# Kernel optimization log

Measured on AMD Instinct MI355X. Metric: run time of the kernel, lower is better.

Reference implementation:

```python
import jax, jax.numpy as jnp
import numpy as np

COMMITMENT_COST = 0.25  # pg_nn.VectorQuantizer default


def setup_inputs() -> dict:
    key = jax.random.key(0)
    k1, k2, k3, k4 = jax.random.split(key, 4)
    B, C, H, W = 32, 128, 64, 64
    D, K = 64, 512
    x = jax.random.normal(k1, (B, C, H, W), jnp.float32)
    # 1x1 conv == per-pixel linear projection; store weight as [D, C]
    conv_w = jax.random.normal(k2, (D, C), jnp.float32) * (1.0 / np.sqrt(C))
    conv_b = jax.random.normal(k3, (D,), jnp.float32) * 0.01
    # VectorQuantizer init: uniform(-1/K, 1/K)
    codebook = jax.random.uniform(k4, (K, D), jnp.float32, -1.0 / K, 1.0 / K)
    return {"x": x, "conv_w": conv_w, "conv_b": conv_b, "codebook": codebook}


def reference(x, conv_w, conv_b, codebook):
    # 1x1 conv projection: [B,C,H,W] -> [B,D,H,W]
    z = jnp.einsum('bchw,dc->bdhw', x, conv_w) + conv_b[None, :, None, None]
    B, D, H, W = z.shape
    flat = z.transpose(0, 2, 3, 1).reshape(-1, D)  # [B*H*W, D]
    # squared L2 distances to each codebook vector: [B*H*W, K]
    dists = (jnp.sum(flat * flat, axis=1, keepdims=True)
             - 2.0 * flat @ codebook.T
             + jnp.sum(codebook * codebook, axis=1))
    idx = jnp.argmin(dists, axis=1)  # [B*H*W]
    quantized = codebook[idx].reshape(B, H, W, D).transpose(0, 3, 1, 2)
    # VQ losses (commitment + embedding)
    commitment = COMMITMENT_COST * jnp.mean(jnp.square(jax.lax.stop_gradient(quantized) - z))
    emb_loss = jnp.mean(jnp.square(quantized - jax.lax.stop_gradient(z)))
    loss = commitment + emb_loss
    # straight-through estimator
    quantized_st = z + jax.lax.stop_gradient(quantized - z)
    return quantized_st, loss
```

## Files before the change

kernel.cpp:

```cpp
#include <hip/hip_runtime.h>
#include <hip/hip_bf16.h>
#include <math.h>

#define CIN   128
#define DDIM  64
#define KCB   512
#define HWSZ  4096
#define NPIX  131072
#define NOUTQ 8388608
#define XPAD  136

typedef short bf16x8 __attribute__((ext_vector_type(8)));
typedef float f32x4  __attribute__((ext_vector_type(4)));
typedef unsigned int u32x2 __attribute__((ext_vector_type(2)));

__device__ __forceinline__ unsigned int bcu(float f){ union{float f;unsigned int u;}v; v.f=f; return v.u; }
__device__ __forceinline__ float bcf(unsigned int u){ union{unsigned int u;float f;}v; v.u=u; return v.f; }
__device__ __forceinline__ unsigned int pkbf(float a, float b){
    union { __hip_bfloat162 h; unsigned int u; } v;
    v.h = __float22bfloat162_rn(make_float2(a, b));
    return v.u;
}

__global__ void vq_zero(float* loss_slot) { *loss_slot = 0.f; }

#define MFMA16(A, B, C) __builtin_amdgcn_mfma_f32_16x16x32_bf16((A), (B), (C), 0, 0, 0)

__device__ __forceinline__ void proj_tile(
    const float (&xr)[32], unsigned short* xrow,
    const unsigned short* sWA, const float* sBias,
    int lg, int klg, int l,
    f32x4& zA, f32x4& zB, f32x4& zC, f32x4& zD, bf16x8& zb0, bf16x8& zb1)
{
    #pragma unroll
    for (int j = 0; j < 8; ++j) {
        u32x2 pv = { pkbf(xr[4*j+0], xr[4*j+1]), pkbf(xr[4*j+2], xr[4*j+3]) };
        *(u32x2*)(xrow + lg * 32 + 4 * j) = pv;
    }
    zA = *(const f32x4*)(sBias +  0 + klg);
    zB = *(const f32x4*)(sBias + 16 + klg);
    zC = *(const f32x4*)(sBias + 32 + klg);
    zD = *(const f32x4*)(sBias + 48 + klg);
    #pragma unroll
    for (int ks = 0; ks < 4; ++ks) {
        bf16x8 xf = *(const bf16x8*)(xrow + ks * 32 + lg * 8);
        bf16x8 w0 = *(const bf16x8*)(sWA + ((0 * 4 + ks) * 64 + l) * 8);
        bf16x8 w1 = *(const bf16x8*)(sWA + ((1 * 4 + ks) * 64 + l) * 8);
        bf16x8 w2 = *(const bf16x8*)(sWA + ((2 * 4 + ks) * 64 + l) * 8);
        bf16x8 w3 = *(const bf16x8*)(sWA + ((3 * 4 + ks) * 64 + l) * 8);
        zA = MFMA16(w0, xf, zA);
        zB = MFMA16(w1, xf, zB);
        zC = MFMA16(w2, xf, zC);
        zD = MFMA16(w3, xf, zD);
    }
    unsigned int* zr = (unsigned int*)xrow;
    u32x2 z0 = { pkbf(zA[0], zA[1]), pkbf(zA[2], zA[3]) };
    u32x2 z1 = { pkbf(zB[0], zB[1]), pkbf(zB[2], zB[3]) };
    u32x2 z2 = { pkbf(zC[0], zC[1]), pkbf(zC[2], zC[3]) };
    u32x2 z3 = { pkbf(zD[0], zD[1]), pkbf(zD[2], zD[3]) };
    *(u32x2*)(zr +  0 + lg * 2) = z0;
    *(u32x2*)(zr +  8 + lg * 2) = z1;
    *(u32x2*)(zr + 16 + lg * 2) = z2;
    *(u32x2*)(zr + 24 + lg * 2) = z3;
    zb0 = *(const bf16x8*)(xrow + lg * 8);
    zb1 = *(const bf16x8*)(xrow + 32 + lg * 8);
}

__global__ __launch_bounds__(1024, 4) void vq_mfma(
    const float* __restrict__ x,
    const float* __restrict__ w,
    const float* __restrict__ bias,
    const float* __restrict__ cb,
    float* __restrict__ out,
    float* __restrict__ loss_slot)
{
    __shared__ __align__(16) unsigned short sCbA[KCB * DDIM];
    __shared__ __align__(16) unsigned short sWA[DDIM * CIN];
    __shared__ __align__(16) float sCbn[KCB];
    __shared__ __align__(16) float sBias[DDIM];
    __shared__ __align__(16) unsigned short sX[16 * 16 * XPAD];
    __shared__ float sLoss[16];

    const int t   = threadIdx.x;
    const int l   = t & 63;
    const int wv  = t >> 6;
    const int p16 = l & 15;
    const int lg  = l >> 4;
    const int klg = lg * 4;

    #pragma unroll
    for (int it = 0; it < 8; ++it) {
        int i = t + it * 1024;
        int k = i >> 4, dg = i & 15;
        f32x4 v = *(const f32x4*)(cb + (size_t)k * DDIM + dg * 4);
        u32x2 pv = { pkbf(-2.f * v[0], -2.f * v[1]), pkbf(-2.f * v[2], -2.f * v[3]) };
        int ct = k >> 4, ks = dg >> 3, lhi = (dg >> 1) & 3, ll = (k & 15) | (lhi << 4);
        *(u32x2*)(sCbA + ((ct * 2 + ks) * 64 + ll) * 8 + (dg & 1) * 4) = pv;
    }
    #pragma unroll
    for (int it = 0; it < 2; ++it) {
        int i = t + it * 1024;
        int d = i >> 5, cg = i & 31;
        f32x4 v = *(const f32x4*)(w + (size_t)d * CIN + cg * 4);
        u32x2 pv = { pkbf(v[0], v[1]), pkbf(v[2], v[3]) };
        int dt = d >> 4, ks = cg >> 3, lhi = (cg >> 1) & 3, ll = (d & 15) | (lhi << 4);
        *(u32x2*)(sWA + ((dt * 4 + ks) * 64 + ll) * 8 + (cg & 1) * 4) = pv;
    }
    if (t < KCB) {
        const f32x4* row = (const f32x4*)(cb + (size_t)t * DDIM);
        float s = 0.f;
        #pragma unroll
        for (int j = 0; j < DDIM / 4; ++j) {
            f32x4 v = row[j];
            s = fmaf(v[0], v[0], s); s = fmaf(v[1], v[1], s);
            s = fmaf(v[2], v[2], s); s = fmaf(v[3], v[3], s);
        }
        sCbn[t] = s;
    }
    if (t < DDIM) sBias[t] = bias[t];
    __syncthreads();

    unsigned short* xrow = sX + wv * (16 * XPAD) + p16 * XPAD;
    const int b   = blockIdx.x >> 3;
    const int hw0 = (blockIdx.x & 7) * 512 + wv * 32;
    const float* xp = x + ((size_t)b * CIN + (size_t)lg * 32) * HWSZ + hw0 + p16;

    float xr0[32], xr1[32];
    #pragma unroll
    for (int j = 0; j < 32; ++j) {
        xr0[j] = xp[(size_t)j * HWSZ];
        xr1[j] = xp[(size_t)j * HWSZ + 16];
    }

    f32x4 zaA0, zaA1, zaA2, zaA3, zaB0, zaB1, zaB2, zaB3;
    bf16x8 zb00, zb01, zb10, zb11;
    proj_tile(xr0, xrow, sWA, sBias, lg, klg, l, zaA0, zaA1, zaA2, zaA3, zb00, zb01);
    proj_tile(xr1, xrow, sWA, sBias, lg, klg, l, zaB0, zaB1, zaB2, zaB3, zb10, zb11);

    float rm00 = INFINITY, rm01 = INFINITY, rm10 = INFINITY, rm11 = INFINITY;
    #pragma unroll 4
    for (int ct = 0; ct < 32; ++ct) {
        f32x4 cinit = *(const f32x4*)(sCbn + ct * 16 + klg);
        bf16x8 c0 = *(const bf16x8*)(sCbA + ((ct * 2 + 0) * 64 + l) * 8);
        bf16x8 c1 = *(const bf16x8*)(sCbA + ((ct * 2 + 1) * 64 + l) * 8);
        f32x4 a0 = MFMA16(c0, zb00, cinit); a0 = MFMA16(c1, zb01, a0);
        f32x4 a1 = MFMA16(c0, zb10, cinit); a1 = MFMA16(c1, zb11, a1);
        unsigned int kb = (unsigned int)(ct * 16 + klg);
        rm00 = fminf(rm00, bcf((bcu(a0[0]) & 0xFFFFFE00u) | (kb + 0)));
        rm01 = fminf(rm01, bcf((bcu(a0[1]) & 0xFFFFFE00u) | (kb + 1)));
        rm00 = fminf(rm00, bcf((bcu(a0[2]) & 0xFFFFFE00u) | (kb + 2)));
        rm01 = fminf(rm01, bcf((bcu(a0[3]) & 0xFFFFFE00u) | (kb + 3)));
        rm10 = fminf(rm10, bcf((bcu(a1[0]) & 0xFFFFFE00u) | (kb + 0)));
        rm11 = fminf(rm11, bcf((bcu(a1[1]) & 0xFFFFFE00u) | (kb + 1)));
        rm10 = fminf(rm10, bcf((bcu(a1[2]) & 0xFFFFFE00u) | (kb + 2)));
        rm11 = fminf(rm11, bcf((bcu(a1[3]) & 0xFFFFFE00u) | (kb + 3)));
    }
    float rn0 = fminf(rm00, rm01);
    rn0 = fminf(rn0, __shfl_xor(rn0, 16, 64));
    rn0 = fminf(rn0, __shfl_xor(rn0, 32, 64));
    const int kbest0 = (int)(bcu(rn0) & 511u);
    float rn1 = fminf(rm10, rm11);
    rn1 = fminf(rn1, __shfl_xor(rn1, 16, 64));
    rn1 = fminf(rn1, __shfl_xor(rn1, 32, 64));
    const int kbest1 = (int)(bcu(rn1) & 511u);

    const float* q0r = cb + (size_t)kbest0 * DDIM;
    const float* q1r = cb + (size_t)kbest1 * DDIM;
    f32x4 qa0 = *(const f32x4*)(q0r +  0 + klg), qb0 = *(const f32x4*)(q1r +  0 + klg);
    f32x4 qa1 = *(const f32x4*)(q0r + 16 + klg), qb1 = *(const f32x4*)(q1r + 16 + klg);
    f32x4 qa2 = *(const f32x4*)(q0r + 32 + klg), qb2 = *(const f32x4*)(q1r + 32 + klg);
    f32x4 qa3 = *(const f32x4*)(q0r + 48 + klg), qb3 = *(const f32x4*)(q1r + 48 + klg);
    float lsum = 0.f;
    size_t ob = ((size_t)b * DDIM + klg) * (size_t)HWSZ + hw0 + p16;
    #pragma unroll
    for (int r = 0; r < 4; ++r) {
        float e;
        e = qa0[r] - zaA0[r]; lsum = fmaf(e, e, lsum);
        e = qb0[r] - zaB0[r]; lsum = fmaf(e, e, lsum);
        e = qa1[r] - zaA1[r]; lsum = fmaf(e, e, lsum);
        e = qb1[r] - zaB1[r]; lsum = fmaf(e, e, lsum);
        e = qa2[r] - zaA2[r]; lsum = fmaf(e, e, lsum);
        e = qb2[r] - zaB2[r]; lsum = fmaf(e, e, lsum);
        e = qa3[r] - zaA3[r]; lsum = fmaf(e, e, lsum);
        e = qb3[r] - zaB3[r]; lsum = fmaf(e, e, lsum);
        out[ob + (size_t)(r +  0) * HWSZ]      = qa0[r];
        out[ob + (size_t)(r +  0) * HWSZ + 16] = qb0[r];
        out[ob + (size_t)(r + 16) * HWSZ]      = qa1[r];
        out[ob + (size_t)(r + 16) * HWSZ + 16] = qb1[r];
        out[ob + (size_t)(r + 32) * HWSZ]      = qa2[r];
        out[ob + (size_t)(r + 32) * HWSZ + 16] = qb2[r];
        out[ob + (size_t)(r + 48) * HWSZ]      = qa3[r];
        out[ob + (size_t)(r + 48) * HWSZ + 16] = qb3[r];
    }

    #pragma unroll
    for (int off = 32; off > 0; off >>= 1)
        lsum += __shfl_down(lsum, off, 64);
    if (l == 0) sLoss[wv] = lsum;
    __syncthreads();
    if (wv == 0) {
        float v = (l < 16) ? sLoss[l] : 0.f;
        v += __shfl_down(v, 8, 64);
        v += __shfl_down(v, 4, 64);
        v += __shfl_down(v, 2, 64);
        v += __shfl_down(v, 1, 64);
        if (l == 0)
            atomicAdd(loss_slot, v * (1.25f / (float)NOUTQ));
    }
}

extern "C" void kernel_launch(void* const* d_in, const int* in_sizes, int n_in,
                              void* d_out, int out_size, void* d_ws, size_t ws_size,
                              hipStream_t stream) {
    const float* x    = (const float*)d_in[0];
    const float* w    = (const float*)d_in[1];
    const float* bias = (const float*)d_in[2];
    const float* cb   = (const float*)d_in[3];
    float* out = (float*)d_out;
    float* loss_slot = out + NOUTQ;

    vq_zero<<<1, 1, 0, stream>>>(loss_slot);
    vq_mfma<<<256, 1024, 0, stream>>>(x, w, bias, cb, out, loss_slot);
}
```

Measured before the change: 49.29 us.

## Split VQ kernel into prep, scan and output kernels via workspace

Replaces the single 256-block fused kernel with three kernels. A prep kernel converts the codebook and weights to bf16 MFMA layout once, in global workspace. A 1024-block scan kernel reads codebook fragments from global/L2 instead of LDS, writes per-pixel indices, and computes the loss from the min distance plus ||z||². A separate output kernel gathers codebook rows and writes the result, reducing the loss partials deterministically. The intent is to remove the per-block LDS staging of the codebook and improve occupancy and parallelism. The cost is two extra launches, an index round trip through memory, and codebook reads in the inner loop served from cache rather than LDS.

```diff
diff --git a/kernel.cpp b/kernel.cpp
--- a/kernel.cpp
+++ b/kernel.cpp
@@ -14,6 +14,12 @@
 typedef float f32x4  __attribute__((ext_vector_type(4)));
 typedef unsigned int u32x2 __attribute__((ext_vector_type(2)));
 
+#define WS_CBA  0
+#define WS_WA   65536
+#define WS_CBN  81920
+#define WS_PART 83968
+#define WS_KB   100352
+
 __device__ __forceinline__ unsigned int bcu(float f){ union{float f;unsigned int u;}v; v.f=f; return v.u; }
 __device__ __forceinline__ float bcf(unsigned int u){ union{unsigned int u;float f;}v; v.u=u; return v.f; }
 __device__ __forceinline__ unsigned int pkbf(float a, float b){
@@ -22,13 +28,44 @@
     return v.u;
 }
 
-__global__ void vq_zero(float* loss_slot) { *loss_slot = 0.f; }
-
 #define MFMA16(A, B, C) __builtin_amdgcn_mfma_f32_16x16x32_bf16((A), (B), (C), 0, 0, 0)
+
+__global__ __launch_bounds__(256) void vq_prep(
+    const float* __restrict__ cb, const float* __restrict__ w,
+    unsigned short* __restrict__ cbA, unsigned short* __restrict__ wA,
+    float* __restrict__ cbn)
+{
+    const int gid = blockIdx.x * 256 + threadIdx.x;
+    {
+        int k = gid >> 4, dg = gid & 15;
+        f32x4 v = *(const f32x4*)(cb + (size_t)k * DDIM + dg * 4);
+        u32x2 pv = { pkbf(-2.f * v[0], -2.f * v[1]), pkbf(-2.f * v[2], -2.f * v[3]) };
+        int ct = k >> 4, ks = dg >> 3, lhi = (dg >> 1) & 3, ll = (k & 15) | (lhi << 4);
+        *(u32x2*)(cbA + ((ct * 2 + ks) * 64 + ll) * 8 + (dg & 1) * 4) = pv;
+    }
+    if (gid < 2048) {
+        int d = gid >> 5, cg = gid & 31;
+        f32x4 v = *(const f32x4*)(w + (size_t)d * CIN + cg * 4);
+        u32x2 pv = { pkbf(v[0], v[1]), pkbf(v[2], v[3]) };
+        int dt = d >> 4, ks = cg >> 3, lhi = (cg >> 1) & 3, ll = (d & 15) | (lhi << 4);
+        *(u32x2*)(wA + ((dt * 4 + ks) * 64 + ll) * 8 + (cg & 1) * 4) = pv;
+    }
+    if (gid < KCB) {
+        const f32x4* row = (const f32x4*)(cb + (size_t)gid * DDIM);
+        float s = 0.f;
+        #pragma unroll
+        for (int j = 0; j < DDIM / 4; ++j) {
+            f32x4 v = row[j];
+            s = fmaf(v[0], v[0], s); s = fmaf(v[1], v[1], s);
+            s = fmaf(v[2], v[2], s); s = fmaf(v[3], v[3], s);
+        }
+        cbn[gid] = s;
+    }
+}
 
 __device__ __forceinline__ void proj_tile(
     const float (&xr)[32], unsigned short* xrow,
-    const unsigned short* sWA, const float* sBias,
+    const unsigned short* __restrict__ wA, const float* __restrict__ bias,
     int lg, int klg, int l,
     f32x4& zA, f32x4& zB, f32x4& zC, f32x4& zD, bf16x8& zb0, bf16x8& zb1)
 {
@@ -37,17 +74,17 @@
         u32x2 pv = { pkbf(xr[4*j+0], xr[4*j+1]), pkbf(xr[4*j+2], xr[4*j+3]) };
         *(u32x2*)(xrow + lg * 32 + 4 * j) = pv;
     }
-    zA = *(const f32x4*)(sBias +  0 + klg);
-    zB = *(const f32x4*)(sBias + 16 + klg);
-    zC = *(const f32x4*)(sBias + 32 + klg);
-    zD = *(const f32x4*)(sBias + 48 + klg);
+    zA = *(const f32x4*)(bias +  0 + klg);
+    zB = *(const f32x4*)(bias + 16 + klg);
+    zC = *(const f32x4*)(bias + 32 + klg);
+    zD = *(const f32x4*)(bias + 48 + klg);
     #pragma unroll
     for (int ks = 0; ks < 4; ++ks) {
         bf16x8 xf = *(const bf16x8*)(xrow + ks * 32 + lg * 8);
-        bf16x8 w0 = *(const bf16x8*)(sWA + ((0 * 4 + ks) * 64 + l) * 8);
-        bf16x8 w1 = *(const bf16x8*)(sWA + ((1 * 4 + ks) * 64 + l) * 8);
-        bf16x8 w2 = *(const bf16x8*)(sWA + ((2 * 4 + ks) * 64 + l) * 8);
-        bf16x8 w3 = *(const bf16x8*)(sWA + ((3 * 4 + ks) * 64 + l) * 8);
+        bf16x8 w0 = *(const bf16x8*)(wA + ((0 * 4 + ks) * 64 + l) * 8);
+        bf16x8 w1 = *(const bf16x8*)(wA + ((1 * 4 + ks) * 64 + l) * 8);
+        bf16x8 w2 = *(const bf16x8*)(wA + ((2 * 4 + ks) * 64 + l) * 8);
+        bf16x8 w3 = *(const bf16x8*)(wA + ((3 * 4 + ks) * 64 + l) * 8);
         zA = MFMA16(w0, xf, zA);
         zB = MFMA16(w1, xf, zB);
         zC = MFMA16(w2, xf, zC);
@@ -66,20 +103,16 @@
     zb1 = *(const bf16x8*)(xrow + 32 + lg * 8);
 }
 
-__global__ __launch_bounds__(1024, 4) void vq_mfma(
+__global__ __launch_bounds__(256, 4) void vq_scan(
     const float* __restrict__ x,
-    const float* __restrict__ w,
     const float* __restrict__ bias,
-    const float* __restrict__ cb,
-    float* __restrict__ out,
-    float* __restrict__ loss_slot)
-{
-    __shared__ __align__(16) unsigned short sCbA[KCB * DDIM];
-    __shared__ __align__(16) unsigned short sWA[DDIM * CIN];
-    __shared__ __align__(16) float sCbn[KCB];
-    __shared__ __align__(16) float sBias[DDIM];
-    __shared__ __align__(16) unsigned short sX[16 * 16 * XPAD];
-    __shared__ float sLoss[16];
+    const unsigned short* __restrict__ cbA,
+    const unsigned short* __restrict__ wA,
+    const float* __restrict__ cbn,
+    unsigned short* __restrict__ kb,
+    float* __restrict__ part)
+{
+    __shared__ __align__(16) unsigned short sX[4 * 16 * XPAD];
 
     const int t   = threadIdx.x;
     const int l   = t & 63;
@@ -88,42 +121,11 @@
     const int lg  = l >> 4;
     const int klg = lg * 4;
 
-    #pragma unroll
-    for (int it = 0; it < 8; ++it) {
-        int i = t + it * 1024;
-        int k = i >> 4, dg = i & 15;
-        f32x4 v = *(const f32x4*)(cb + (size_t)k * DDIM + dg * 4);
-        u32x2 pv = { pkbf(-2.f * v[0], -2.f * v[1]), pkbf(-2.f * v[2], -2.f * v[3]) };
-        int ct = k >> 4, ks = dg >> 3, lhi = (dg >> 1) & 3, ll = (k & 15) | (lhi << 4);
-        *(u32x2*)(sCbA + ((ct * 2 + ks) * 64 + ll) * 8 + (dg & 1) * 4) = pv;
-    }
-    #pragma unroll
-    for (int it = 0; it < 2; ++it) {
-        int i = t + it * 1024;
-        int d = i >> 5, cg = i & 31;
-        f32x4 v = *(const f32x4*)(w + (size_t)d * CIN + cg * 4);
-        u32x2 pv = { pkbf(v[0], v[1]), pkbf(v[2], v[3]) };
-        int dt = d >> 4, ks = cg >> 3, lhi = (cg >> 1) & 3, ll = (d & 15) | (lhi << 4);
-        *(u32x2*)(sWA + ((dt * 4 + ks) * 64 + ll) * 8 + (cg & 1) * 4) = pv;
-    }
-    if (t < KCB) {
-        const f32x4* row = (const f32x4*)(cb + (size_t)t * DDIM);
-        float s = 0.f;
-        #pragma unroll
-        for (int j = 0; j < DDIM / 4; ++j) {
-            f32x4 v = row[j];
-            s = fmaf(v[0], v[0], s); s = fmaf(v[1], v[1], s);
-            s = fmaf(v[2], v[2], s); s = fmaf(v[3], v[3], s);
-        }
-        sCbn[t] = s;
-    }
-    if (t < DDIM) sBias[t] = bias[t];
-    __syncthreads();
-
+    const int pixg = blockIdx.x * 128 + wv * 32;
+    const int b   = pixg >> 12;
+    const int hw0 = pixg & 4095;
+    const float* xp = x + ((size_t)b * CIN + (size_t)lg * 32) * HWSZ + hw0 + p16;
     unsigned short* xrow = sX + wv * (16 * XPAD) + p16 * XPAD;
-    const int b   = blockIdx.x >> 3;
-    const int hw0 = (blockIdx.x & 7) * 512 + wv * 32;
-    const float* xp = x + ((size_t)b * CIN + (size_t)lg * 32) * HWSZ + hw0 + p16;
 
     float xr0[32], xr1[32];
     #pragma unroll
@@ -134,26 +136,26 @@
 
     f32x4 zaA0, zaA1, zaA2, zaA3, zaB0, zaB1, zaB2, zaB3;
     bf16x8 zb00, zb01, zb10, zb11;
-    proj_tile(xr0, xrow, sWA, sBias, lg, klg, l, zaA0, zaA1, zaA2, zaA3, zb00, zb01);
-    proj_tile(xr1, xrow, sWA, sBias, lg, klg, l, zaB0, zaB1, zaB2, zaB3, zb10, zb11);
+    proj_tile(xr0, xrow, wA, bias, lg, klg, l, zaA0, zaA1, zaA2, zaA3, zb00, zb01);
+    proj_tile(xr1, xrow, wA, bias, lg, klg, l, zaB0, zaB1, zaB2, zaB3, zb10, zb11);
 
     float rm00 = INFINITY, rm01 = INFINITY, rm10 = INFINITY, rm11 = INFINITY;
     #pragma unroll 4
     for (int ct = 0; ct < 32; ++ct) {
-        f32x4 cinit = *(const f32x4*)(sCbn + ct * 16 + klg);
-        bf16x8 c0 = *(const bf16x8*)(sCbA + ((ct * 2 + 0) * 64 + l) * 8);
-        bf16x8 c1 = *(const bf16x8*)(sCbA + ((ct * 2 + 1) * 64 + l) * 8);
+        f32x4 cinit = *(const f32x4*)(cbn + ct * 16 + klg);
+        bf16x8 c0 = *(const bf16x8*)(cbA + ((ct * 2 + 0) * 64 + l) * 8);
+        bf16x8 c1 = *(const bf16x8*)(cbA + ((ct * 2 + 1) * 64 + l) * 8);
         f32x4 a0 = MFMA16(c0, zb00, cinit); a0 = MFMA16(c1, zb01, a0);
         f32x4 a1 = MFMA16(c0, zb10, cinit); a1 = MFMA16(c1, zb11, a1);
-        unsigned int kb = (unsigned int)(ct * 16 + klg);
-        rm00 = fminf(rm00, bcf((bcu(a0[0]) & 0xFFFFFE00u) | (kb + 0)));
-        rm01 = fminf(rm01, bcf((bcu(a0[1]) & 0xFFFFFE00u) | (kb + 1)));
-        rm00 = fminf(rm00, bcf((bcu(a0[2]) & 0xFFFFFE00u) | (kb + 2)));
-        rm01 = fminf(rm01, bcf((bcu(a0[3]) & 0xFFFFFE00u) | (kb + 3)));
-        rm10 = fminf(rm10, bcf((bcu(a1[0]) & 0xFFFFFE00u) | (kb + 0)));
-        rm11 = fminf(rm11, bcf((bcu(a1[1]) & 0xFFFFFE00u) | (kb + 1)));
-        rm10 = fminf(rm10, bcf((bcu(a1[2]) & 0xFFFFFE00u) | (kb + 2)));
-        rm11 = fminf(rm11, bcf((bcu(a1[3]) & 0xFFFFFE00u) | (kb + 3)));
+        unsigned int kbse = (unsigned int)(ct * 16 + klg);
+        rm00 = fminf(rm00, bcf((bcu(a0[0]) & 0xFFFFFE00u) | (kbse + 0)));
+        rm01 = fminf(rm01, bcf((bcu(a0[1]) & 0xFFFFFE00u) | (kbse + 1)));
+        rm00 = fminf(rm00, bcf((bcu(a0[2]) & 0xFFFFFE00u) | (kbse + 2)));
+        rm01 = fminf(rm01, bcf((bcu(a0[3]) & 0xFFFFFE00u) | (kbse + 3)));
+        rm10 = fminf(rm10, bcf((bcu(a1[0]) & 0xFFFFFE00u) | (kbse + 0)));
+        rm11 = fminf(rm11, bcf((bcu(a1[1]) & 0xFFFFFE00u) | (kbse + 1)));
+        rm10 = fminf(rm10, bcf((bcu(a1[2]) & 0xFFFFFE00u) | (kbse + 2)));
+        rm11 = fminf(rm11, bcf((bcu(a1[3]) & 0xFFFFFE00u) | (kbse + 3)));
     }
     float rn0 = fminf(rm00, rm01);
     rn0 = fminf(rn0, __shfl_xor(rn0, 16, 64));
@@ -164,48 +166,57 @@
     rn1 = fminf(rn1, __shfl_xor(rn1, 32, 64));
     const int kbest1 = (int)(bcu(rn1) & 511u);
 
-    const float* q0r = cb + (size_t)kbest0 * DDIM;
-    const float* q1r = cb + (size_t)kbest1 * DDIM;
-    f32x4 qa0 = *(const f32x4*)(q0r +  0 + klg), qb0 = *(const f32x4*)(q1r +  0 + klg);
-    f32x4 qa1 = *(const f32x4*)(q0r + 16 + klg), qb1 = *(const f32x4*)(q1r + 16 + klg);
-    f32x4 qa2 = *(const f32x4*)(q0r + 32 + klg), qb2 = *(const f32x4*)(q1r + 32 + klg);
-    f32x4 qa3 = *(const f32x4*)(q0r + 48 + klg), qb3 = *(const f32x4*)(q1r + 48 + klg);
-    float lsum = 0.f;
-    size_t ob = ((size_t)b * DDIM + klg) * (size_t)HWSZ + hw0 + p16;
+    float zn0 = 0.f, zn1 = 0.f;
     #pragma unroll
     for (int r = 0; r < 4; ++r) {
-        float e;
-        e = qa0[r] - zaA0[r]; lsum = fmaf(e, e, lsum);
-        e = qb0[r] - zaB0[r]; lsum = fmaf(e, e, lsum);
-        e = qa1[r] - zaA1[r]; lsum = fmaf(e, e, lsum);
-        e = qb1[r] - zaB1[r]; lsum = fmaf(e, e, lsum);
-        e = qa2[r] - zaA2[r]; lsum = fmaf(e, e, lsum);
-        e = qb2[r] - zaB2[r]; lsum = fmaf(e, e, lsum);
-        e = qa3[r] - zaA3[r]; lsum = fmaf(e, e, lsum);
-        e = qb3[r] - zaB3[r]; lsum = fmaf(e, e, lsum);
-        out[ob + (size_t)(r +  0) * HWSZ]      = qa0[r];
-        out[ob + (size_t)(r +  0) * HWSZ + 16] = qb0[r];
-        out[ob + (size_t)(r + 16) * HWSZ]      = qa1[r];
-        out[ob + (size_t)(r + 16) * HWSZ + 16] = qb1[r];
-        out[ob + (size_t)(r + 32) * HWSZ]      = qa2[r];
-        out[ob + (size_t)(r + 32) * HWSZ + 16] = qb2[r];
-        out[ob + (size_t)(r + 48) * HWSZ]      = qa3[r];
-        out[ob + (size_t)(r + 48) * HWSZ + 16] = qb3[r];
-    }
-
+        zn0 = fmaf(zaA0[r], zaA0[r], zn0); zn0 = fmaf(zaA1[r], zaA1[r], zn0);
+        zn0 = fmaf(zaA2[r], zaA2[r], zn0); zn0 = fmaf(zaA3[r], zaA3[r], zn0);
+        zn1 = fmaf(zaB0[r], zaB0[r], zn1); zn1 = fmaf(zaB1[r], zaB1[r], zn1);
+        zn1 = fmaf(zaB2[r], zaB2[r], zn1); zn1 = fmaf(zaB3[r], zaB3[r], zn1);
+    }
+    zn0 += __shfl_xor(zn0, 16, 64); zn0 += __shfl_xor(zn0, 32, 64);
+    zn1 += __shfl_xor(zn1, 16, 64); zn1 += __shfl_xor(zn1, 32, 64);
+
+    if (l < 16) {
+        kb[pixg + p16]      = (unsigned short)kbest0;
+        kb[pixg + 16 + p16] = (unsigned short)kbest1;
+    }
+    float lv = 0.25f * ((rn0 + zn0) + (rn1 + zn1));
     #pragma unroll
     for (int off = 32; off > 0; off >>= 1)
-        lsum += __shfl_down(lsum, off, 64);
-    if (l == 0) sLoss[wv] = lsum;
-    __syncthreads();
-    if (wv == 0) {
-        float v = (l < 16) ? sLoss[l] : 0.f;
-        v += __shfl_down(v, 8, 64);
-        v += __shfl_down(v, 4, 64);
-        v += __shfl_down(v, 2, 64);
-        v += __shfl_down(v, 1, 64);
-        if (l == 0)
-            atomicAdd(loss_slot, v * (1.25f / (float)NOUTQ));
+        lv += __shfl_down(lv, off, 64);
+    if (l == 0) part[blockIdx.x * 4 + wv] = lv;
+}
+
+__global__ __launch_bounds__(256, 8) void vq_out(
+    const float* __restrict__ cb, const unsigned short* __restrict__ kb,
+    const float* __restrict__ part, float* __restrict__ out,
+    float* __restrict__ loss_slot)
+{
+    const int t   = threadIdx.x;
+    const int bid = blockIdx.x;
+    const int px  = ((bid >> 2) << 8) + t;
+    const int dq  = bid & 3;
+    const int b   = px >> 12;
+    const int hw  = px & 4095;
+    const int k   = kb[px];
+    const f32x4* qr = (const f32x4*)(cb + (size_t)k * DDIM + dq * 16);
+    f32x4 q0 = qr[0], q1 = qr[1], q2 = qr[2], q3 = qr[3];
+    size_t base = ((size_t)b * DDIM + dq * 16) * (size_t)HWSZ + hw;
+    #pragma unroll
+    for (int r = 0; r < 4; ++r) {
+        out[base + (size_t)(r +  0) * HWSZ] = q0[r];
+        out[base + (size_t)(r +  4) * HWSZ] = q1[r];
+        out[base + (size_t)(r +  8) * HWSZ] = q2[r];
+        out[base + (size_t)(r + 12) * HWSZ] = q3[r];
+    }
+    if (bid == 0 && t < 64) {
+        float s = 0.f;
+        #pragma unroll
+        for (int j = 0; j < 64; ++j) s += part[t + j * 64];
+        #pragma unroll
+        for (int off = 32; off > 0; off >>= 1) s += __shfl_down(s, off, 64);
+        if (t == 0) *loss_slot = s * (1.25f / (float)NOUTQ);
     }
 }
 
@@ -219,6 +230,14 @@
     float* out = (float*)d_out;
     float* loss_slot = out + NOUTQ;
 
-    vq_zero<<<1, 1, 0, stream>>>(loss_slot);
-    vq_mfma<<<256, 1024, 0, stream>>>(x, w, bias, cb, out, loss_slot);
-}
+    char* ws = (char*)d_ws;
+    unsigned short* cbA = (unsigned short*)(ws + WS_CBA);
+    unsigned short* wA  = (unsigned short*)(ws + WS_WA);
+    float*          cbn = (float*)(ws + WS_CBN);
+    float*          prt = (float*)(ws + WS_PART);
+    unsigned short* kbb = (unsigned short*)(ws + WS_KB);
+
+    vq_prep<<<32,   256, 0, stream>>>(cb, w, cbA, wA, cbn);
+    vq_scan<<<1024, 256, 0, stream>>>(x, bias, cbA, wA, cbn, kbb, prt);
+    vq_out <<<2048, 256, 0, stream>>>(cb, kbb, prt, out, loss_slot);
+}
```

Measured after the change: 67.20 us. +36.4%, slower.
